# Kernel optimization log

Measured on AMD Instinct MI355X. Metric: run time of the kernel, lower is better.

The kernel has to match this reference:

```python
import jax, jax.numpy as jnp
import numpy as np

D = 256   # koopman_dim
B = 256   # batch of initial latent states
T_STEPS = 512
DT = 0.01


def setup_inputs() -> dict:
    key = jax.random.key(0)
    k1, k2 = jax.random.split(key)
    z0 = jax.random.normal(k1, (B, D), dtype=jnp.float32)
    # nnx.Linear default lecun_normal init: std ~ 1/sqrt(fan_in)
    kernel = jax.random.normal(k2, (D, D), dtype=jnp.float32) / jnp.sqrt(jnp.float32(D))
    log_dt = jnp.asarray(jnp.log(DT), dtype=jnp.float32)
    return {"z0": z0, "kernel": kernel, "log_dt": log_dt, "T": T_STEPS}


def reference(z0, kernel, log_dt, T):
    dt = jnp.exp(log_dt)
    eye = jnp.eye(kernel.shape[0], dtype=kernel.dtype)
    # Bilinear / Tustin discretization: K_d = (I - 0.5*dt*K)^-1 (I + 0.5*dt*K)
    K_discrete = jnp.linalg.solve(eye - 0.5 * dt * kernel, eye + 0.5 * dt * kernel)

    def step(z, _):
        z_next = z @ K_discrete  # [B, D] @ [D, D]
        return z_next, z_next

    _, preds = jax.lax.scan(step, z0, None, length=T)  # preds: [T, B, D]
    return jnp.transpose(preds, (1, 0, 2))  # [B, T, D]
```

## Files before the change

### kernel.cpp

```cpp
#include <hip/hip_runtime.h>


#define DD 256
#define TT 512
#define MATF (DD * DD)
#define LDT ((size_t)TT * (size_t)DD)

typedef __attribute__((ext_vector_type(8))) short bf16x8;
typedef __attribute__((ext_vector_type(4))) float f32x4;

#define GLD16(g, l)                                                  \
    __builtin_amdgcn_global_load_lds(                                \
        (const __attribute__((address_space(1))) void*)(g),          \
        (__attribute__((address_space(3))) void*)(l), 16, 0, 0)

static __device__ __forceinline__ unsigned short f2bf(float f) {
    unsigned int u = __float_as_uint(f);
    u += 0x7fffu + ((u >> 16) & 1u);
    return (unsigned short)(u >> 16);
}
static __device__ __forceinline__ unsigned pack2bf(float a, float b) {
    return (unsigned)f2bf(a) | ((unsigned)f2bf(b) << 16);
}

__device__ __forceinline__ void g32_core(const float* __restrict__ Ab, int lda,
                                         const float* __restrict__ Bb, int ldb,
                                         int rowBase, int colBase, float acc[2][2]) {
    __shared__ __align__(16) float As[64 * 38];
    __shared__ __align__(16) float Bs[64 * 40];
    const int tid = threadIdx.x;
    const int tx = tid & 15, ty = tid >> 4;
    const int am = tid >> 4;
    const int ak = (tid & 15) << 2;
    const int bk = tid >> 3;
    const int bn = (tid & 7) << 2;

    acc[0][0] = acc[0][1] = acc[1][0] = acc[1][1] = 0.f;

    float4 pa0 = *(const float4*)(Ab + (size_t)(rowBase + am) * lda + ak);
    float4 pa1 = *(const float4*)(Ab + (size_t)(rowBase + am + 16) * lda + ak);
    float4 pb0 = *(const float4*)(Bb + (size_t)bk * ldb + colBase + bn);
    float4 pb1 = *(const float4*)(Bb + (size_t)(bk + 32) * ldb + colBase + bn);

    for (int k0 = 0; k0 < DD; k0 += 64) {
        As[(ak + 0) * 38 + am] = pa0.x;
        As[(ak + 1) * 38 + am] = pa0.y;
        As[(ak + 2) * 38 + am] = pa0.z;
        As[(ak + 3) * 38 + am] = pa0.w;
        As[(ak + 0) * 38 + am + 16] = pa1.x;
        As[(ak + 1) * 38 + am + 16] = pa1.y;
        As[(ak + 2) * 38 + am + 16] = pa1.z;
        As[(ak + 3) * 38 + am + 16] = pa1.w;
        *(float4*)(&Bs[bk * 40 + bn]) = pb0;
        *(float4*)(&Bs[(bk + 32) * 40 + bn]) = pb1;
        __syncthreads();
        if (k0 + 64 < DD) {
            pa0 = *(const float4*)(Ab + (size_t)(rowBase + am) * lda + k0 + 64 + ak);
            pa1 = *(const float4*)(Ab + (size_t)(rowBase + am + 16) * lda + k0 + 64 + ak);
            pb0 = *(const float4*)(Bb + (size_t)(bk + k0 + 64) * ldb + colBase + bn);
            pb1 = *(const float4*)(Bb + (size_t)(bk + 32 + k0 + 64) * ldb + colBase + bn);
        }
#pragma unroll
        for (int kk = 0; kk < 64; ++kk) {
            float2 a2 = *(const float2*)(&As[kk * 38 + (ty << 1)]);
            float2 b2 = *(const float2*)(&Bs[kk * 40 + (tx << 1)]);
            acc[0][0] = fmaf(a2.x, b2.x, acc[0][0]);
            acc[0][1] = fmaf(a2.x, b2.y, acc[0][1]);
            acc[1][0] = fmaf(a2.y, b2.x, acc[1][0]);
            acc[1][1] = fmaf(a2.y, b2.y, acc[1][1]);
        }
        __syncthreads();
    }
}

__global__ void __launch_bounds__(256)
n1_kernel(const float* __restrict__ K, const float* __restrict__ log_dt,
          const float* __restrict__ z0, float* __restrict__ A2,
          float* __restrict__ Bop, unsigned short* __restrict__ Zb0) {
    const float cs = 0.5f * expf(log_dt[0]);
    {
        int b = ((blockIdx.y * 8 + blockIdx.x) * 256 + threadIdx.x) * 4;
        uint2 w;
        w.x = pack2bf(z0[b], z0[b + 1]);
        w.y = pack2bf(z0[b + 2], z0[b + 3]);
        *(uint2*)(Zb0 + b) = w;
    }
    float acc[2][2];
    const int rowBase = blockIdx.y << 5, colBase = blockIdx.x << 5;
    g32_core(K, DD, K, DD, rowBase, colBase, acc);
    const float cs2 = cs * cs;
    const int r0 = rowBase + ((threadIdx.x >> 4) << 1);
    const int c0 = colBase + ((threadIdx.x & 15) << 1);
#pragma unroll
    for (int i = 0; i < 2; ++i) {
        int r = r0 + i;
        float e0 = K[(size_t)r * DD + c0], e1 = K[(size_t)r * DD + c0 + 1];
        float p0 = cs2 * acc[i][0], p1 = cs2 * acc[i][1];
        *(float2*)(A2 + (size_t)r * DD + c0) = (float2){p0, p1};
        float2 w;
        w.x = 2.f * p0 + 2.f * cs * e0 + (r == c0 ? 2.f : 0.f);
        w.y = 2.f * p1 + 2.f * cs * e1 + (r == c0 + 1 ? 2.f : 0.f);
        *(float2*)(Bop + (size_t)r * DD + c0) = w;
    }
}

__global__ void __launch_bounds__(256)
n2_kernel(const float* __restrict__ A2, const float* __restrict__ Bop,
          const float* __restrict__ K, const float* __restrict__ log_dt,
          float* __restrict__ E) {
    const float cs = 0.5f * expf(log_dt[0]);
    float acc[2][2];
    const int rowBase = blockIdx.y << 5, colBase = blockIdx.x << 5;
    g32_core(A2, DD, Bop, DD, rowBase, colBase, acc);
    const int r0 = rowBase + ((threadIdx.x >> 4) << 1);
    const int c0 = colBase + ((threadIdx.x & 15) << 1);
#pragma unroll
    for (int i = 0; i < 2; ++i) {
        int r = r0 + i;
        float e0 = K[(size_t)r * DD + c0], e1 = K[(size_t)r * DD + c0 + 1];
        float2 v;
        v.x = acc[i][0] + 2.f * cs * e0;
        v.y = acc[i][1] + 2.f * cs * e1;
        *(float2*)(E + (size_t)r * DD + c0) = v;
    }
}

__global__ void __launch_bounds__(256)
gpow_kernel(const float* __restrict__ A, const float* __restrict__ B,
            float* __restrict__ C, long long sA, long long sB, long long sC) {
    float acc[2][2];
    const int rowBase = blockIdx.y << 5, colBase = blockIdx.x << 5;
    g32_core(A + blockIdx.z * sA, DD, B + blockIdx.z * sB, DD, rowBase, colBase, acc);
    float* Cb = C + blockIdx.z * sC;
    const int r0 = rowBase + ((threadIdx.x >> 4) << 1);
    const int c0 = colBase + ((threadIdx.x & 15) << 1);
#pragma unroll
    for (int i = 0; i < 2; ++i) {
        int r = r0 + i;
        *(float2*)(Cb + (size_t)r * DD + c0) = (float2){acc[i][0], acc[i][1]};
    }
}

__global__ void __launch_bounds__(256)
comb_kernel(const float* __restrict__ Epow, unsigned short* __restrict__ MTb,
            float* __restrict__ W1) {
    __shared__ float tle[6][32][33];
    const int tid = threadIdx.x;
    const int k0 = blockIdx.y << 5, c0 = blockIdx.x << 5;
    const int ltx = tid & 31, lty = tid >> 5;
#pragma unroll
    for (int m = 0; m < 6; ++m)
#pragma unroll
        for (int it = 0; it < 4; ++it) {
            int k = lty + (it << 3);
            tle[m][ltx][k] =
                Epow[(size_t)m * MATF + (size_t)(k0 + k) * DD + c0 + ltx];
        }
    __syncthreads();

    const int c = tid >> 3;
    const int kb = (tid & 7) << 2;
    float em[6][4];
#pragma unroll
    for (int m = 0; m < 6; ++m)
#pragma unroll
        for (int u = 0; u < 4; ++u) em[m][u] = tle[m][c][kb + u];

    float w32[4];
    for (int j = 1; j <= 32; ++j) {
        float val[4];
#pragma unroll
        for (int u = 0; u < 4; ++u)
            val[u] = ((k0 + kb + u) == (c0 + c)) ? 1.f : 0.f;
        int coef = 1;
#pragma unroll
        for (int m = 1; m <= 6; ++m) {
            coef = coef * (j - m + 1) / m;
            float cf = (float)(coef < 0 ? 0 : coef);
#pragma unroll
            for (int u = 0; u < 4; ++u) val[u] = fmaf(cf, em[m - 1][u], val[u]);
        }
        uint2 w;
        w.x = pack2bf(val[0], val[1]);
        w.y = pack2bf(val[2], val[3]);
        *(uint2*)(MTb + (size_t)(j - 1) * MATF + (size_t)(c0 + c) * DD + k0 + kb) = w;
        if (j == 32) {
            w32[0] = val[0]; w32[1] = val[1]; w32[2] = val[2]; w32[3] = val[3];
        }
    }
    __syncthreads();
    float* tw = &tle[0][0][0];
#pragma unroll
    for (int u = 0; u < 4; ++u) tw[(kb + u) * 33 + c] = w32[u];
    __syncthreads();
    const int wk = tid >> 3, wc = (tid & 7) << 2;
    float4 v = {tw[wk * 33 + wc], tw[wk * 33 + wc + 1], tw[wk * 33 + wc + 2],
                tw[wk * 33 + wc + 3]};
    *(float4*)(W1 + (size_t)(k0 + wk) * DD + c0 + wc) = v;
}

__global__ void __launch_bounds__(256)
scan_kernel(const float* __restrict__ z0, float* __restrict__ out,
            const float* __restrict__ W1, float* __restrict__ Wtab,
            unsigned short* __restrict__ Zb, int s) {
    const int nvec = 1 << s;
    const int mm = blockIdx.z;
    const float* W = (s == 0) ? W1 : Wtab + (size_t)(s - 1) * MATF;
    float acc[2][2];
    const int rowBase = blockIdx.y << 5, colBase = blockIdx.x << 5;
    const int r0 = rowBase + ((threadIdx.x >> 4) << 1);
    const int c0 = colBase + ((threadIdx.x & 15) << 1);
    if (mm < nvec) {
        const float* Asrc = mm ? out + (size_t)(32 * mm - 1) * DD : z0;
        int lda = mm ? (int)LDT : DD;
        g32_core(Asrc, lda, W, DD, rowBase, colBase, acc);
        const int dst = nvec + mm;
        float* Of = out + (size_t)(32 * dst - 1) * DD;
        unsigned short* Zo = Zb + (size_t)dst * MATF;
#pragma unroll
        for (int ii = 0; ii < 2; ++ii) {
            int r = r0 + ii;
            float2 v = {acc[ii][0], acc[ii][1]};
            *(float2*)(Of + (size_t)r * LDT + c0) = v;
            *(unsigned*)(Zo + (size_t)r * DD + c0) = pack2bf(v.x, v.y);
        }
    } else {
        g32_core(W, DD, W, DD, rowBase, colBase, acc);
        float* Cb = Wtab + (size_t)s * MATF;
#pragma unroll
        for (int ii = 0; ii < 2; ++ii) {
            int r = r0 + ii;
            *(float2*)(Cb + (size_t)r * DD + c0) = (float2){acc[ii][0], acc[ii][1]};
        }
    }
}

__global__ void __launch_bounds__(256)
fill_kernel(const unsigned short* __restrict__ Zb,
            const unsigned short* __restrict__ MTb,
            float* __restrict__ out) {
    __shared__ __align__(16) char pool[32768];
    const int bz = blockIdx.z;
    const int i = (bz >= 465) ? 15 : bz / 31;
    const int j = bz - i * 31 + 1;
    const int t = i * 32 + j - 1;
    const unsigned short* Zt = Zb + (size_t)i * MATF;
    const unsigned short* MT = MTb + (size_t)(j - 1) * MATF;

    const int tid = threadIdx.x;
    const int lane = tid & 63, wid = tid >> 6;
    const int rowBase = blockIdx.y * 128, colBase = blockIdx.x * 128;
    const int wr = (wid >> 1) * 64, wc = (wid & 1) * 64;

    int rowq[4], skq[4], ldsb[4];
#pragma unroll
    for (int q = 0; q < 4; ++q) {
        int c = q * 256 + wid * 64 + lane;
        int row = c >> 3;
        rowq[q] = row;
        skq[q] = ((c ^ (row & 7)) & 7) << 3;
        ldsb[q] = (q * 256 + wid * 64) << 4;
    }

    f32x4 acc[4][4];
#pragma unroll
    for (int a = 0; a < 4; ++a)
#pragma unroll
        for (int b = 0; b < 4; ++b) acc[a][b] = (f32x4){0.f, 0.f, 0.f, 0.f};

    auto stage = [&](int k0) {
#pragma unroll
        for (int q = 0; q < 4; ++q) {
            GLD16(Zt + (size_t)(rowBase + rowq[q]) * DD + k0 + skq[q], pool + ldsb[q]);
            GLD16(MT + (size_t)(colBase + rowq[q]) * DD + k0 + skq[q],
                  pool + 16384 + ldsb[q]);
        }
    };

    stage(0);
    for (int r = 0; r < 4; ++r) {
        __syncthreads();
        const char* asb = pool;
        const char* bsb = pool + 16384;
#pragma unroll
        for (int ks = 0; ks < 2; ++ks) {
            bf16x8 af[4], bg[4];
            const int kk = ks * 32 + (lane >> 4) * 8;
#pragma unroll
            for (int f = 0; f < 4; ++f) {
                int rr = wr + f * 16 + (lane & 15);
                af[f] = *(const bf16x8*)(asb + ((rr * 128 + kk * 2) ^ ((rr & 7) << 4)));
                int cc = wc + f * 16 + (lane & 15);
                bg[f] = *(const bf16x8*)(bsb + ((cc * 128 + kk * 2) ^ ((cc & 7) << 4)));
            }
#pragma unroll
            for (int fr = 0; fr < 4; ++fr)
#pragma unroll
                for (int fc = 0; fc < 4; ++fc)
                    acc[fr][fc] = __builtin_amdgcn_mfma_f32_16x16x32_bf16(
                        af[fr], bg[fc], acc[fr][fc], 0, 0, 0);
        }
        __syncthreads();
        if (r < 3) stage((r + 1) * 64);
    }

    float* Cs = (float*)pool;
    float* C = out + (size_t)t * DD;
#pragma unroll
    for (int hp = 0; hp < 2; ++hp) {
        __syncthreads();
        if (wr == hp * 64) {
#pragma unroll
            for (int fr = 0; fr < 4; ++fr) {
#pragma unroll
                for (int fc = 0; fc < 4; ++fc) {
                    int ccol = wc + fc * 16 + (lane & 15);
#pragma unroll
                    for (int ii = 0; ii < 4; ++ii) {
                        int lr = fr * 16 + ((lane >> 4) << 2) + ii;
                        int csw = ccol ^ (((lr >> 2) & 1) << 4);
                        Cs[lr * 128 + csw] = acc[fr][fc][ii];
                    }
                }
            }
        }
        __syncthreads();
#pragma unroll
        for (int it = 0; it < 8; ++it) {
            int chunk = it * 256 + tid;
            int row = chunk >> 5;
            int c4 = (chunk & 31) << 2;
            int csw = c4 ^ (((row >> 2) & 1) << 4);
            float4 v = *(const float4*)(Cs + row * 128 + csw);
            *(float4*)(C + (size_t)(rowBase + hp * 64 + row) * LDT + colBase + c4) = v;
        }
    }
}

__global__ void prep_kernel(const float* __restrict__ K,
                            const float* __restrict__ log_dt,
                            float* __restrict__ A) {
    int idx = blockIdx.x * blockDim.x + threadIdx.x;
    A[idx] = 0.5f * expf(log_dt[0]) * K[idx];
}

template <int EPI>
__global__ void __launch_bounds__(256)
g32_kernel(const float* A, const float* B, float* C, const float* E, float* C2,
           int lda, int ldb, int ldc, long long sA, long long sB, long long sC) {
    float acc[2][2];
    const int rowBase = blockIdx.y << 5, colBase = blockIdx.x << 5;
    g32_core(A + blockIdx.z * sA, lda, B + blockIdx.z * sB, ldb, rowBase, colBase, acc);
    float* Cb = C + blockIdx.z * sC;
    const int r0 = rowBase + ((threadIdx.x >> 4) << 1);
    const int c0 = colBase + ((threadIdx.x & 15) << 1);
#pragma unroll
    for (int i = 0; i < 2; ++i) {
        int r = r0 + i;
        float2 v;
        if (EPI == 2) {
            float e0 = E[(size_t)r * DD + c0], e1 = E[(size_t)r * DD + c0 + 1];
            v.x = acc[i][0] + 2.f * e0 + (r == c0 ? 1.f : 0.f);
            v.y = acc[i][1] + 2.f * e1 + (r == c0 + 1 ? 1.f : 0.f);
        } else {
            v.x = acc[i][0];
            v.y = acc[i][1];
        }
        *(float2*)(Cb + (size_t)r * ldc + c0) = v;
        if (EPI == 1) {
            float e0 = E[(size_t)r * DD + c0], e1 = E[(size_t)r * DD + c0 + 1];
            float2 w;
            w.x = 2.f * acc[i][0] + 2.f * e0 + (r == c0 ? 2.f : 0.f);
            w.y = 2.f * acc[i][1] + 2.f * e1 + (r == c0 + 1 ? 2.f : 0.f);
            *(float2*)(C2 + (size_t)r * DD + c0) = w;
        }
    }
}

extern "C" void kernel_launch(void* const* d_in, const int* in_sizes, int n_in,
                              void* d_out, int out_size, void* d_ws, size_t ws_size,
                              hipStream_t stream) {
    const float* z0 = (const float*)d_in[0];
    const float* Kmat = (const float*)d_in[1];
    const float* log_dt = (const float*)d_in[2];
    float* out = (float*)d_out;

    dim3 blk(256);

    float* A2 = (float*)d_ws;
    float* Bop = A2 + MATF;
    float* Epow = Bop + MATF;
    float* W1 = Epow + (size_t)6 * MATF;
    float* Wtab = W1 + MATF;
    unsigned short* MTb = (unsigned short*)(Wtab + (size_t)3 * MATF);
    unsigned short* Zb = MTb + (size_t)32 * MATF;
    const size_t need = (size_t)12 * MATF * 4 + (size_t)48 * MATF * 2;

    if (ws_size >= need) {
        dim3 g(8, 8, 1);
        n1_kernel<<<g, blk, 0, stream>>>(Kmat, log_dt, z0, A2, Bop, Zb);
        n2_kernel<<<g, blk, 0, stream>>>(A2, Bop, Kmat, log_dt, Epow);

        gpow_kernel<<<g, blk, 0, stream>>>(Epow, Epow, Epow + MATF, 0, 0, 0);
        gpow_kernel<<<dim3(8, 8, 2), blk, 0, stream>>>(
            Epow, Epow + MATF, Epow + 2 * (size_t)MATF, MATF, 0, MATF);
        gpow_kernel<<<dim3(8, 8, 2), blk, 0, stream>>>(
            Epow + MATF, Epow + 2 * (size_t)MATF, Epow + 4 * (size_t)MATF,
            MATF, 0, MATF);

        comb_kernel<<<g, blk, 0, stream>>>(Epow, MTb, W1);

        const int njobs[4] = {2, 3, 5, 8};
        for (int s = 0; s < 4; ++s)
            scan_kernel<<<dim3(8, 8, njobs[s]), blk, 0, stream>>>(
                z0, out, W1, Wtab, Zb, s);

        fill_kernel<<<dim3(2, 2, 497), blk, 0, stream>>>(Zb, MTb, out);
        return;
    }

    float* A = (float*)d_ws;
    float* A2f = A + MATF;
    float* Bopf = A2f + MATF;
    float* Kd = Bopf + MATF;
    prep_kernel<<<MATF / 256, blk, 0, stream>>>(Kmat, log_dt, A);
    dim3 g(8, 8, 1);
    g32_kernel<1><<<g, blk, 0, stream>>>(A, A, A2f, A, Bopf, DD, DD, DD, 0, 0, 0);
    g32_kernel<2><<<g, blk, 0, stream>>>(A2f, Bopf, Kd, A, (float*)0, DD, DD, DD, 0, 0, 0);
    for (int t = 0; t < TT; ++t) {
        const float* Ain = (t == 0) ? z0 : out + (size_t)(t - 1) * DD;
        int lda = (t == 0) ? DD : (int)LDT;
        g32_kernel<0><<<g, blk, 0, stream>>>(Ain, Kd, out + (size_t)t * DD,
                                             (const float*)0, (float*)0,
                                             lda, DD, (int)LDT, 0, 0, 0);
    }
}
```

Measured before the change: 120.5 us.

## Compute K^32/K^64/K^96 via binomial series and shorten scan to three levels

Extends the power-series expansion of the discrete operator to eighth order so that comb_kernel directly produces the 32-, 64- and 96-step propagators alongside the per-step tables. This lets the block-level scan over 16 chunk states run in three dependent launches instead of four, with a table-driven job list that mixes state propagation and propagator squaring. Two extra high-order powers are computed in one batched gpow launch instead of one. The intent is to cut serial kernel launches on the critical path, at the cost of more matrix-power work and reliance on series truncation accuracy for larger step counts.

Result: no change. 120.0 us (-0.4%).

```diff
diff --git a/kernel.cpp b/kernel.cpp
--- a/kernel.cpp
+++ b/kernel.cpp
@@ -142,14 +142,35 @@
 }
 
 __global__ void __launch_bounds__(256)
+gpow4_kernel(float* __restrict__ Epow) {
+    static const int sa[4] = {1, 2, 2, 3};
+    static const int sb[4] = {2, 2, 3, 3};
+    static const int sc[4] = {4, 5, 6, 7};
+    const int z = blockIdx.z;
+    float acc[2][2];
+    const int rowBase = blockIdx.y << 5, colBase = blockIdx.x << 5;
+    g32_core(Epow + (size_t)sa[z] * MATF, DD, Epow + (size_t)sb[z] * MATF, DD,
+             rowBase, colBase, acc);
+    float* Cb = Epow + (size_t)sc[z] * MATF;
+    const int r0 = rowBase + ((threadIdx.x >> 4) << 1);
+    const int c0 = colBase + ((threadIdx.x & 15) << 1);
+#pragma unroll
+    for (int i = 0; i < 2; ++i) {
+        int r = r0 + i;
+        *(float2*)(Cb + (size_t)r * DD + c0) = (float2){acc[i][0], acc[i][1]};
+    }
+}
+
+__global__ void __launch_bounds__(256)
 comb_kernel(const float* __restrict__ Epow, unsigned short* __restrict__ MTb,
-            float* __restrict__ W1) {
-    __shared__ float tle[6][32][33];
+            float* __restrict__ W1, float* __restrict__ W2,
+            float* __restrict__ W3) {
+    __shared__ float tle[8][32][33];
     const int tid = threadIdx.x;
     const int k0 = blockIdx.y << 5, c0 = blockIdx.x << 5;
     const int ltx = tid & 31, lty = tid >> 5;
 #pragma unroll
-    for (int m = 0; m < 6; ++m)
+    for (int m = 0; m < 8; ++m)
 #pragma unroll
         for (int it = 0; it < 4; ++it) {
             int k = lty + (it << 3);
@@ -160,21 +181,23 @@
 
     const int c = tid >> 3;
     const int kb = (tid & 7) << 2;
-    float em[6][4];
-#pragma unroll
-    for (int m = 0; m < 6; ++m)
+    float em[8][4];
+#pragma unroll
+    for (int m = 0; m < 8; ++m)
 #pragma unroll
         for (int u = 0; u < 4; ++u) em[m][u] = tle[m][c][kb + u];
+
+    float diag[4];
+#pragma unroll
+    for (int u = 0; u < 4; ++u)
+        diag[u] = ((k0 + kb + u) == (c0 + c)) ? 1.f : 0.f;
 
     float w32[4];
     for (int j = 1; j <= 32; ++j) {
-        float val[4];
-#pragma unroll
-        for (int u = 0; u < 4; ++u)
-            val[u] = ((k0 + kb + u) == (c0 + c)) ? 1.f : 0.f;
-        int coef = 1;
-#pragma unroll
-        for (int m = 1; m <= 6; ++m) {
+        float val[4] = {diag[0], diag[1], diag[2], diag[3]};
+        long long coef = 1;
+#pragma unroll
+        for (int m = 1; m <= 8; ++m) {
             coef = coef * (j - m + 1) / m;
             float cf = (float)(coef < 0 ? 0 : coef);
 #pragma unroll
@@ -188,35 +211,71 @@
             w32[0] = val[0]; w32[1] = val[1]; w32[2] = val[2]; w32[3] = val[3];
         }
     }
-    __syncthreads();
+    float w64[4] = {diag[0], diag[1], diag[2], diag[3]};
+    float w96[4] = {diag[0], diag[1], diag[2], diag[3]};
+    {
+        double c64 = 1.0, c96 = 1.0;
+#pragma unroll
+        for (int m = 1; m <= 8; ++m) {
+            c64 = c64 * (double)(64 - m + 1) / (double)m;
+            c96 = c96 * (double)(96 - m + 1) / (double)m;
+            float f64 = (float)c64, f96 = (float)c96;
+#pragma unroll
+            for (int u = 0; u < 4; ++u) {
+                w64[u] = fmaf(f64, em[m - 1][u], w64[u]);
+                w96[u] = fmaf(f96, em[m - 1][u], w96[u]);
+            }
+        }
+    }
     float* tw = &tle[0][0][0];
-#pragma unroll
-    for (int u = 0; u < 4; ++u) tw[(kb + u) * 33 + c] = w32[u];
-    __syncthreads();
     const int wk = tid >> 3, wc = (tid & 7) << 2;
-    float4 v = {tw[wk * 33 + wc], tw[wk * 33 + wc + 1], tw[wk * 33 + wc + 2],
-                tw[wk * 33 + wc + 3]};
-    *(float4*)(W1 + (size_t)(k0 + wk) * DD + c0 + wc) = v;
-}
-
-__global__ void __launch_bounds__(256)
-scan_kernel(const float* __restrict__ z0, float* __restrict__ out,
-            const float* __restrict__ W1, float* __restrict__ Wtab,
-            unsigned short* __restrict__ Zb, int s) {
-    const int nvec = 1 << s;
-    const int mm = blockIdx.z;
-    const float* W = (s == 0) ? W1 : Wtab + (size_t)(s - 1) * MATF;
-    float acc[2][2];
-    const int rowBase = blockIdx.y << 5, colBase = blockIdx.x << 5;
-    const int r0 = rowBase + ((threadIdx.x >> 4) << 1);
-    const int c0 = colBase + ((threadIdx.x & 15) << 1);
-    if (mm < nvec) {
-        const float* Asrc = mm ? out + (size_t)(32 * mm - 1) * DD : z0;
-        int lda = mm ? (int)LDT : DD;
-        g32_core(Asrc, lda, W, DD, rowBase, colBase, acc);
-        const int dst = nvec + mm;
-        float* Of = out + (size_t)(32 * dst - 1) * DD;
-        unsigned short* Zo = Zb + (size_t)dst * MATF;
+    float* Wd[3] = {W1, W2, W3};
+    float* Ws[3] = {w32, w64, w96};
+#pragma unroll
+    for (int p = 0; p < 3; ++p) {
+        __syncthreads();
+#pragma unroll
+        for (int u = 0; u < 4; ++u) tw[(kb + u) * 33 + c] = Ws[p][u];
+        __syncthreads();
+        float4 v = {tw[wk * 33 + wc], tw[wk * 33 + wc + 1],
+                    tw[wk * 33 + wc + 2], tw[wk * 33 + wc + 3]};
+        *(float4*)(Wd[p] + (size_t)(k0 + wk) * DD + c0 + wc) = v;
+    }
+}
+
+__global__ void __launch_bounds__(256)
+scan3_kernel(const float* __restrict__ z0, float* __restrict__ out,
+             const float* __restrict__ W1, const float* __restrict__ W2,
+             const float* __restrict__ W3, float* __restrict__ Wtab,
+             unsigned short* __restrict__ Zb, int level) {
+    static const signed char JA[3][7] = {{0, 0, 0, 17, 18, 0, 0},
+                                         {0, 1, 2, 3, 2, 3, 20},
+                                         {4, 5, 0, 1, 2, 3, 0}};
+    static const signed char JB[3][7] = {{0, 1, 2, 1, 2, 0, 0},
+                                         {3, 3, 3, 3, 4, 4, 4},
+                                         {4, 4, 5, 5, 5, 5, 0}};
+    static const signed char JD[3][7] = {{1, 2, 3, 19, 20, 0, 0},
+                                         {4, 5, 6, 7, 8, 9, 21},
+                                         {10, 11, 12, 13, 14, 15, 0}};
+    const float* Wp[6] = {W1, W2, W3, Wtab, Wtab + MATF, Wtab + 2 * (size_t)MATF};
+    const int jz = blockIdx.z;
+    const int a = JA[level][jz], b = JB[level][jz], d = JD[level][jz];
+
+    const float* Asrc;
+    int lda;
+    if (a == 0) { Asrc = z0; lda = DD; }
+    else if (a < 16) { Asrc = out + (size_t)(32 * a - 1) * DD; lda = (int)LDT; }
+    else { Asrc = Wp[a - 16]; lda = DD; }
+
+    float acc[2][2];
+    const int rowBase = blockIdx.y << 5, colBase = blockIdx.x << 5;
+    g32_core(Asrc, lda, Wp[b], DD, rowBase, colBase, acc);
+
+    const int r0 = rowBase + ((threadIdx.x >> 4) << 1);
+    const int c0 = colBase + ((threadIdx.x & 15) << 1);
+    if (d < 16) {
+        float* Of = out + (size_t)(32 * d - 1) * DD;
+        unsigned short* Zo = Zb + (size_t)d * MATF;
 #pragma unroll
         for (int ii = 0; ii < 2; ++ii) {
             int r = r0 + ii;
@@ -225,8 +284,7 @@
             *(unsigned*)(Zo + (size_t)r * DD + c0) = pack2bf(v.x, v.y);
         }
     } else {
-        g32_core(W, DD, W, DD, rowBase, colBase, acc);
-        float* Cb = Wtab + (size_t)s * MATF;
+        float* Cb = Wtab + (size_t)(d - 19) * MATF;
 #pragma unroll
         for (int ii = 0; ii < 2; ++ii) {
             int r = r0 + ii;
@@ -390,11 +448,13 @@
     float* A2 = (float*)d_ws;
     float* Bop = A2 + MATF;
     float* Epow = Bop + MATF;
-    float* W1 = Epow + (size_t)6 * MATF;
-    float* Wtab = W1 + MATF;
+    float* W1 = Epow + (size_t)8 * MATF;
+    float* W2 = W1 + MATF;
+    float* W3 = W2 + MATF;
+    float* Wtab = W3 + MATF;
     unsigned short* MTb = (unsigned short*)(Wtab + (size_t)3 * MATF);
     unsigned short* Zb = MTb + (size_t)32 * MATF;
-    const size_t need = (size_t)12 * MATF * 4 + (size_t)48 * MATF * 2;
+    const size_t need = (size_t)16 * MATF * 4 + (size_t)48 * MATF * 2;
 
     if (ws_size >= need) {
         dim3 g(8, 8, 1);
@@ -404,16 +464,14 @@
         gpow_kernel<<<g, blk, 0, stream>>>(Epow, Epow, Epow + MATF, 0, 0, 0);
         gpow_kernel<<<dim3(8, 8, 2), blk, 0, stream>>>(
             Epow, Epow + MATF, Epow + 2 * (size_t)MATF, MATF, 0, MATF);
-        gpow_kernel<<<dim3(8, 8, 2), blk, 0, stream>>>(
-            Epow + MATF, Epow + 2 * (size_t)MATF, Epow + 4 * (size_t)MATF,
-            MATF, 0, MATF);
-
-        comb_kernel<<<g, blk, 0, stream>>>(Epow, MTb, W1);
-
-        const int njobs[4] = {2, 3, 5, 8};
-        for (int s = 0; s < 4; ++s)
-            scan_kernel<<<dim3(8, 8, njobs[s]), blk, 0, stream>>>(
-                z0, out, W1, Wtab, Zb, s);
+        gpow4_kernel<<<dim3(8, 8, 4), blk, 0, stream>>>(Epow);
+
+        comb_kernel<<<g, blk, 0, stream>>>(Epow, MTb, W1, W2, W3);
+
+        const int njobs[3] = {5, 7, 6};
+        for (int s = 0; s < 3; ++s)
+            scan3_kernel<<<dim3(8, 8, njobs[s]), blk, 0, stream>>>(
+                z0, out, W1, W2, W3, Wtab, Zb, s);
 
         fill_kernel<<<dim3(2, 2, 497), blk, 0, stream>>>(Zb, MTb, out);
         return;
```
